# Kernel tuning notes

Hardware: AMD Instinct MI355X
Metric: run time of the kernel (lower is better)

Reference implementation:

```python
import jax, jax.numpy as jnp
import numpy as np

B, S, E, H = 2, 2048, 1024, 16
D = E // H  # head_dim
SCALE = 1.0 / np.sqrt(D)


def rope_tables(seq_len, dim, dtype=jnp.float32):
    # matches RotaryEmbedding: inv_freq over even indices, emb = cat([freqs, freqs])
    inv_freq = 1.0 / (10000.0 ** (jnp.arange(0, dim, 2, dtype=dtype) / dim))
    t = jnp.arange(seq_len, dtype=dtype)
    freqs = t[:, None] * inv_freq[None, :]          # [S, D/2]
    emb = jnp.concatenate([freqs, freqs], axis=-1)  # [S, D]
    return jnp.cos(emb)[None, None], jnp.sin(emb)[None, None]  # [1,1,S,D]


def apply_rope(x, cos, sin):
    # x: [B,H,S,D]; interleaved rotate exactly as the torch code:
    # x2 = stack([-x[...,1::2], x[...,0::2]], -1).reshape_as(x)
    x2 = jnp.stack([-x[..., 1::2], x[..., 0::2]], axis=-1).reshape(x.shape)
    return x * cos + x2 * sin


def setup_inputs() -> dict:
    key = jax.random.key(0)
    ks = jax.random.split(key, 12)
    std = 1.0 / np.sqrt(E)
    inp = {
        "query": jax.random.normal(ks[0], (B, S, E), jnp.float32),
        "key": jax.random.normal(ks[1], (B, S, E), jnp.float32),
        "value": jax.random.normal(ks[2], (B, S, E), jnp.float32),
        "mask": jnp.ones((B, S), jnp.int32),
        "Wq": jax.random.normal(ks[3], (E, E), jnp.float32) * std,
        "bq": jax.random.normal(ks[4], (E,), jnp.float32) * std,
        "Wk": jax.random.normal(ks[5], (E, E), jnp.float32) * std,
        "bk": jax.random.normal(ks[6], (E,), jnp.float32) * std,
        "Wv": jax.random.normal(ks[7], (E, E), jnp.float32) * std,
        "bv": jax.random.normal(ks[8], (E,), jnp.float32) * std,
        "Wo": jax.random.normal(ks[9], (E, E), jnp.float32) * std,
        "bo": jax.random.normal(ks[10], (E,), jnp.float32) * std,
    }
    return inp


def reference(query, key, value, mask, Wq, bq, Wk, bk, Wv, bv, Wo, bo):
    b, sq, _ = query.shape
    sk = key.shape[1]
    # linear projections (torch Linear: x @ W.T + b), split into heads [B,H,S,D]
    Q = (query @ Wq.T + bq).reshape(b, sq, H, D).transpose(0, 2, 1, 3)
    K = (key @ Wk.T + bk).reshape(b, sk, H, D).transpose(0, 2, 1, 3)
    V = (value @ Wv.T + bv).reshape(b, sk, H, D).transpose(0, 2, 1, 3)
    cos_q, sin_q = rope_tables(sq, D)
    cos_k, sin_k = rope_tables(sk, D)
    Q = apply_rope(Q, cos_q, sin_q)
    K = apply_rope(K, cos_k, sin_k)
    scores = jnp.einsum("bhqd,bhkd->bhqk", Q, K) * SCALE
    neg_inf = jnp.finfo(scores.dtype).min
    scores = jnp.where(mask[:, None, None, :] == 0, neg_inf, scores)
    attn = jax.nn.softmax(scores, axis=-1)
    # dropout omitted (deterministic reference / eval mode)
    out = jnp.einsum("bhqk,bhkd->bhqd", attn, V)
    out = out.transpose(0, 2, 1, 3).reshape(b, sq, E)
    return out @ Wo.T + bo
```

## Files before the change

### kernel.cpp

```cpp
#include <hip/hip_runtime.h>
#include <stdint.h>

typedef unsigned short u16;
typedef __bf16 bf16x8 __attribute__((ext_vector_type(8)));
typedef float f32x4 __attribute__((ext_vector_type(4)));
typedef float f32x2 __attribute__((ext_vector_type(2)));
typedef u16 u16x4v __attribute__((ext_vector_type(4)));

#define DI __device__ __forceinline__

constexpr int BB = 2, SS = 2048, EE = 1024, HH = 16, DD = 64;
constexpr int MROWS = BB * SS;
constexpr int KDIM = 1024, NDIM = 1024;

constexpr float FM = 12.0f;
constexpr float MNEG = -30000.f;

DI u16 f2bf(float f) {
  uint32_t u = __float_as_uint(f);
  return (u16)((u + 0x7FFFu + ((u >> 16) & 1u)) >> 16);
}
DI float bf2f(u16 h) { return __uint_as_float(((uint32_t)h) << 16); }

DI uint32_t cvtpk_bf16(float a, float b) {
  uint32_t r;
  asm("v_cvt_pk_bf16_f32 %0, %1, %2" : "=v"(r) : "v"(a), "v"(b));
  return r;
}

DI void cp16(const void* g, void* lds) {
  __builtin_amdgcn_global_load_lds((const __attribute__((address_space(1))) void*)g,
                                   (__attribute__((address_space(3))) void*)lds, 16, 0, 0);
}

DI f32x4 mfma16(bf16x8 a, bf16x8 b, f32x4 c) {
  return __builtin_amdgcn_mfma_f32_16x16x32_bf16(a, b, c, 0, 0, 0);
}

__global__ __launch_bounds__(256) void prep_cast(
    const float* __restrict__ q, const float* __restrict__ k, const float* __restrict__ v,
    const float* __restrict__ wq, const float* __restrict__ wk, const float* __restrict__ wv,
    const float* __restrict__ wo,
    u16* __restrict__ qb, u16* __restrict__ kb, u16* __restrict__ vb,
    u16* __restrict__ wqb, u16* __restrict__ wkb, u16* __restrict__ wvb,
    u16* __restrict__ wob) {
  constexpr size_t SZI = (size_t)MROWS * EE;
  constexpr size_t SZW = (size_t)EE * EE;
  const size_t g = ((size_t)blockIdx.x * 256 + threadIdx.x) * 4;
  const float* src; u16* dst; size_t o;
  if (g < SZI)          { src = q; dst = qb; o = g; }
  else if (g < 2 * SZI) { src = k; dst = kb; o = g - SZI; }
  else if (g < 3 * SZI) { src = v; dst = vb; o = g - 2 * SZI; }
  else {
    size_t t2 = g - 3 * SZI;
    int wi = (int)(t2 / SZW);
    o = t2 - (size_t)(wi < 4 ? wi : 3) * SZW;
    src = wi == 0 ? wq : wi == 1 ? wk : wi == 2 ? wv : wo;
    dst = wi == 0 ? wqb : wi == 1 ? wkb : wi == 2 ? wvb : wob;
  }
  const float4 f = *(const float4*)(src + o);
  u16x4v hv;
  hv[0] = f2bf(f.x); hv[1] = f2bf(f.y); hv[2] = f2bf(f.z); hv[3] = f2bf(f.w);
  *(u16x4v*)(dst + o) = hv;
}

__global__ __launch_bounds__(256) void rope_tables_k(float* __restrict__ csT,
                                                     const int* __restrict__ mask,
                                                     float* __restrict__ mfl) {
  const int t = blockIdx.x * 256 + threadIdx.x;
  const int s = t >> 6, d = t & 63, j = d & 31;
  const float ang = (float)s * exp2f(-(float)j * 0.4152410118f);
  float2 cs; cs.x = cosf(ang); cs.y = sinf(ang);
  ((float2*)csT)[t] = cs;
  if (t < BB * SS) mfl[t] = mask[t] ? -FM : MNEG;
}

__global__ __launch_bounds__(256) void gemm_qkv(
    const u16* __restrict__ qb, const u16* __restrict__ kb, const u16* __restrict__ vb,
    const u16* __restrict__ wqb, const u16* __restrict__ wkb, const u16* __restrict__ wvb,
    const float* __restrict__ bq, const float* __restrict__ bk, const float* __restrict__ bv,
    u16* __restrict__ Qp, u16* __restrict__ Kp, u16* __restrict__ Vtg,
    const float* __restrict__ csT) {
  __shared__ alignas(16) u16 sA[2][128 * 64];
  __shared__ alignas(16) u16 sB[2][128 * 64];
  const int tsel = blockIdx.y >> 5;
  const bool vtr = (tsel == 2);
  const u16* A    = tsel == 0 ? wqb : tsel == 1 ? wkb : vb;
  const u16* Bm   = tsel == 0 ? qb  : tsel == 1 ? kb  : wvb;
  const float* bias = tsel == 0 ? bq : tsel == 1 ? bk : bv;

  const int fBase = blockIdx.x * 128;
  const int tBase = (blockIdx.y & 31) * 128;
  const int aBase = vtr ? tBase : fBase;
  const int bBase = vtr ? fBase : tBase;
  const int tid = threadIdx.x;
  const int lane = tid & 63, w = tid >> 6;
  const int quad = lane >> 4, l16 = lane & 15;
  const int wr = w >> 1, wc = w & 1;

  size_t aSrc[4], bSrc[4];
  int dOff[4];
#pragma unroll
  for (int j = 0; j < 4; ++j) {
    const int c = tid + j * 256;
    const int row = c >> 3, sl = c & 7;
    const size_t off = (size_t)row * KDIM + ((sl ^ (row & 7)) * 8);
    aSrc[j] = (size_t)aBase * KDIM + off;
    bSrc[j] = (size_t)bBase * KDIM + off;
    dOff[j] = c * 8;
  }

  f32x4 acc[4][4];
#pragma unroll
  for (int mi = 0; mi < 4; ++mi)
#pragma unroll
    for (int ni = 0; ni < 4; ++ni)
#pragma unroll
      for (int e = 0; e < 4; ++e) acc[mi][ni][e] = 0.f;

  const int arow = wr * 64 + l16, brow = wc * 64 + l16;

  auto stage = [&](int k0, int bi) {
#pragma unroll
    for (int j = 0; j < 4; ++j) {
      cp16(A + aSrc[j] + k0, &sA[bi][dOff[j]]);
      cp16(Bm + bSrc[j] + k0, &sB[bi][dOff[j]]);
    }
  };

  stage(0, 0);
  __syncthreads();
  int buf = 0;
  for (int k0 = 0; k0 < KDIM; k0 += 64) {
    if (k0 + 64 < KDIM) stage(k0 + 64, buf ^ 1);
    __builtin_amdgcn_s_setprio(1);
#pragma unroll
    for (int h = 0; h < 2; ++h) {
      bf16x8 af[4], bf[4];
#pragma unroll
      for (int i = 0; i < 4; ++i) {
        const int ar = arow + i * 16, br = brow + i * 16;
        af[i] = *(const bf16x8*)&sA[buf][ar * 64 + (((h * 4 + quad) ^ (ar & 7)) << 3)];
        bf[i] = *(const bf16x8*)&sB[buf][br * 64 + (((h * 4 + quad) ^ (br & 7)) << 3)];
      }
#pragma unroll
      for (int mi = 0; mi < 4; ++mi)
#pragma unroll
        for (int ni = 0; ni < 4; ++ni)
          acc[mi][ni] = mfma16(af[mi], bf[ni], acc[mi][ni]);
    }
    __builtin_amdgcn_s_setprio(0);
    __syncthreads();
    buf ^= 1;
  }

  if (!vtr) {
    u16* C = tsel == 0 ? Qp : Kp;
#pragma unroll
    for (int mi = 0; mi < 4; ++mi) {
      const int fm = fBase + wr * 64 + mi * 16 + quad * 4;
      const float4 b4 = *(const float4*)&bias[fm];
      const int d0 = fm & 63;
#pragma unroll
      for (int ni = 0; ni < 4; ++ni) {
        const int t = tBase + wc * 64 + ni * 16 + l16;
        const int srow = t & (SS - 1);
        const float* cs = &csT[(size_t)((srow << 6) + d0) * 2];
        const float4 cs01 = *(const float4*)cs;
        const float4 cs23 = *(const float4*)(cs + 4);
        const float v0 = acc[mi][ni][0] + b4.x;
        const float v1 = acc[mi][ni][1] + b4.y;
        const float v2 = acc[mi][ni][2] + b4.z;
        const float v3 = acc[mi][ni][3] + b4.w;
        const float o0 = v0 * cs01.x - v1 * cs01.y;
        const float o1 = v1 * cs01.z + v0 * cs01.w;
        const float o2 = v2 * cs23.x - v3 * cs23.y;
        const float o3 = v3 * cs23.z + v2 * cs23.w;
        uint2 pk;
        pk.x = cvtpk_bf16(o0, o1);
        pk.y = cvtpk_bf16(o2, o3);
        *(uint2*)&C[(size_t)t * NDIM + fm] = pk;
      }
    }
  } else {
#pragma unroll
    for (int ni = 0; ni < 4; ++ni) {
      const int f = fBase + wc * 64 + ni * 16 + l16;
      const int h = f >> 6, d = f & 63;
      const float bb = bias[f];
#pragma unroll
      for (int mi = 0; mi < 4; ++mi) {
        const int t0 = tBase + wr * 64 + mi * 16 + quad * 4;
        const int b = t0 >> 11, s0 = t0 & (SS - 1);
        const int sp0 = (s0 & ~31) | (((s0 >> 2) & 3) << 3) | (((s0 >> 4) & 1) << 2);
        uint2 pk;
        pk.x = cvtpk_bf16(acc[mi][ni][0] + bb, acc[mi][ni][1] + bb);
        pk.y = cvtpk_bf16(acc[mi][ni][2] + bb, acc[mi][ni][3] + bb);
        *(uint2*)&Vtg[((size_t)((b * 16 + h) * 64 + d)) * SS + sp0] = pk;
      }
    }
  }
}

__global__ __launch_bounds__(512, 4) void attn_kernel(
    const u16* __restrict__ Qp, const u16* __restrict__ Kp, const u16* __restrict__ Vtg,
    const float* __restrict__ mfl, u16* __restrict__ Oh) {
  __shared__ alignas(16) u16 sK[2][128 * 64];
  __shared__ alignas(16) u16 sVt[2][64 * 128];
  __shared__ alignas(16) float sMaskAll[SS];
  const int tid = threadIdx.x, lane = tid & 63, w = tid >> 6;
  const int quad = lane >> 4, l16 = lane & 15;
  const int bh = blockIdx.y, b = bh >> 4, h = bh & 15;
  const int q0 = blockIdx.x * 128 + w * 16;
  const u16* Qb = Qp + (size_t)b * SS * EE + h * DD;
  const u16* Kb = Kp + (size_t)b * SS * EE + h * DD;
  const u16* Vb = Vtg + (size_t)bh * DD * SS;
  constexpr float C1 = 0.18033688011112042f;

  bf16x8 qf[2];
#pragma unroll
  for (int ks = 0; ks < 2; ++ks)
    qf[ks] = *(const bf16x8*)(Qb + (size_t)(q0 + l16) * EE + ks * 32 + quad * 8);

  f32x4 oacc[4];
#pragma unroll
  for (int nd = 0; nd < 4; ++nd)
#pragma unroll
    for (int e = 0; e < 4; ++e) oacc[nd][e] = 0.f;
  f32x2 sum2 = {0.f, 0.f};

  auto stage = [&](int kt, int bi) {
    const int key0 = kt * 128;
#pragma unroll
    for (int i = 0; i < 2; ++i) {
      const int c = i * 512 + tid;
      const int key = c >> 3;
      const int g8 = ((c & 7) ^ (key & 7)) * 8;
      cp16(Kb + (size_t)(key0 + key) * EE + g8, &sK[bi][c * 8]);
    }
#pragma unroll
    for (int i = 0; i < 2; ++i) {
      const int L = i * 512 + tid;
      const int d = L >> 4;
      const int g8 = ((L & 15) ^ (d & 15)) * 8;
      cp16(Vb + (size_t)d * SS + key0 + g8, &sVt[bi][L * 8]);
    }
  };

  auto compute = [&](int kt, int bi) {
    const int key0 = kt * 128;
    f32x4 sacc[8];
#pragma unroll
    for (int ni = 0; ni < 8; ++ni)
#pragma unroll
      for (int e = 0; e < 4; ++e) sacc[ni][e] = 0.f;
    __builtin_amdgcn_s_setprio(1);
#pragma unroll
    for (int ks = 0; ks < 2; ++ks)
#pragma unroll
      for (int ni = 0; ni < 8; ++ni) {
        const int row = ni * 16 + l16;
        const bf16x8 kf = *(const bf16x8*)&sK[bi][row * 64 + (((ks * 4 + quad) ^ (l16 & 7)) << 3)];
        sacc[ni] = mfma16(kf, qf[ks], sacc[ni]);
      }
    __builtin_amdgcn_s_setprio(0);

    uint32_t pw32[4][4];
#pragma unroll
    for (int ni = 0; ni < 8; ++ni) {
      const int kb4 = key0 + ni * 16 + quad * 4;
      const f32x2 m01 = *(const f32x2*)&sMaskAll[kb4];
      const f32x2 m23 = *(const f32x2*)&sMaskAll[kb4 + 2];
      f32x2 t01, t23;
      t01.x = sacc[ni][0]; t01.y = sacc[ni][1];
      t23.x = sacc[ni][2]; t23.y = sacc[ni][3];
      t01 = t01 * C1 + m01;
      t23 = t23 * C1 + m23;
      f32x2 p01, p23;
      p01.x = __builtin_amdgcn_exp2f(t01.x); p01.y = __builtin_amdgcn_exp2f(t01.y);
      p23.x = __builtin_amdgcn_exp2f(t23.x); p23.y = __builtin_amdgcn_exp2f(t23.y);
      sum2 += p01;
      sum2 += p23;
      const int k2 = ni >> 1, j2 = (ni & 1) * 2;
      pw32[k2][j2]     = cvtpk_bf16(p01.x, p01.y);
      pw32[k2][j2 + 1] = cvtpk_bf16(p23.x, p23.y);
    }

    __builtin_amdgcn_s_setprio(1);
#pragma unroll
    for (int k2 = 0; k2 < 4; ++k2) {
      union { uint32_t u[4]; bf16x8 v; } pf;
#pragma unroll
      for (int j = 0; j < 4; ++j) pf.u[j] = pw32[k2][j];
#pragma unroll
      for (int nd = 0; nd < 4; ++nd) {
        const int row = nd * 16 + l16;
        const bf16x8 vf = *(const bf16x8*)&sVt[bi][row * 128 + (((k2 * 4 + quad) ^ l16) << 3)];
        oacc[nd] = mfma16(pf.v, vf, oacc[nd]);
      }
    }
    __builtin_amdgcn_s_setprio(0);
  };

  stage(0, 0);
  cp16(mfl + (size_t)b * SS + tid * 4, &sMaskAll[tid * 4]);
  __syncthreads();

  for (int kt = 0; kt < SS / 128; kt += 2) {
    if (kt + 1 < SS / 128) stage(kt + 1, 1);
    compute(kt, 0);
    __syncthreads();
    if (kt + 2 < SS / 128) stage(kt + 2, 0);
    compute(kt + 1, 1);
    __syncthreads();
  }

  float lrow = sum2.x + sum2.y;
  lrow += __shfl_xor(lrow, 16, 64);
  lrow += __shfl_xor(lrow, 32, 64);
  const float linv = lrow > 0.f ? 1.0f / lrow : 0.f;

#pragma unroll
  for (int r = 0; r < 4; ++r) {
    const float li = __shfl(linv, quad * 4 + r, 16);
    const size_t row = (size_t)(b * SS + q0 + quad * 4 + r) * EE + h * DD;
#pragma unroll
    for (int nd = 0; nd < 4; ++nd) {
      const int d = nd * 16 + l16;
      Oh[row + d] = f2bf(oacc[nd][r] * li);
    }
  }
}

__global__ __launch_bounds__(256) void gemm_out(
    const u16* __restrict__ Ab, const u16* __restrict__ Bb,
    const float* __restrict__ bias, float* __restrict__ Cout) {
  __shared__ alignas(16) u16 sA[2][128 * 64];
  __shared__ alignas(16) u16 sB[2][64 * 64];
  const int rowBase = blockIdx.y * 128;
  const int colBase = blockIdx.x * 64;
  const int tid = threadIdx.x;
  const int lane = tid & 63, w = tid >> 6;
  const int quad = lane >> 4, l16 = lane & 15;
  const int wr = w >> 1, wc = w & 1;

  size_t aSrc[4]; int aOff[4];
  size_t bSrc[2]; int bOff[2];
#pragma unroll
  for (int j = 0; j < 4; ++j) {
    const int c = tid + j * 256;
    const int row = c >> 3, sl = c & 7;
    aSrc[j] = (size_t)(rowBase + row) * KDIM + ((sl ^ (row & 7)) * 8);
    aOff[j] = c * 8;
  }
#pragma unroll
  for (int j = 0; j < 2; ++j) {
    const int c = tid + j * 256;
    const int row = c >> 3, sl = c & 7;
    bSrc[j] = (size_t)(colBase + row) * KDIM + ((sl ^ (row & 7)) * 8);
    bOff[j] = c * 8;
  }

  f32x4 acc[4][2];
#pragma unroll
  for (int mi = 0; mi < 4; ++mi)
#pragma unroll
    for (int ni = 0; ni < 2; ++ni)
#pragma unroll
      for (int e = 0; e < 4; ++e) acc[mi][ni][e] = 0.f;

  const int arow = wr * 64 + l16, brow = wc * 32 + l16;

  auto stage = [&](int k0, int bi) {
#pragma unroll
    for (int j = 0; j < 4; ++j) cp16(Ab + aSrc[j] + k0, &sA[bi][aOff[j]]);
#pragma unroll
    for (int j = 0; j < 2; ++j) cp16(Bb + bSrc[j] + k0, &sB[bi][bOff[j]]);
  };

  stage(0, 0);
  __syncthreads();
  int buf = 0;
  for (int k0 = 0; k0 < KDIM; k0 += 64) {
    if (k0 + 64 < KDIM) stage(k0 + 64, buf ^ 1);
    __builtin_amdgcn_s_setprio(1);
#pragma unroll
    for (int h = 0; h < 2; ++h) {
      bf16x8 af[4], bf[2];
#pragma unroll
      for (int i = 0; i < 4; ++i) {
        const int ar = arow + i * 16;
        af[i] = *(const bf16x8*)&sA[buf][ar * 64 + (((h * 4 + quad) ^ (ar & 7)) << 3)];
      }
#pragma unroll
      for (int i = 0; i < 2; ++i) {
        const int br = brow + i * 16;
        bf[i] = *(const bf16x8*)&sB[buf][br * 64 + (((h * 4 + quad) ^ (br & 7)) << 3)];
      }
#pragma unroll
      for (int mi = 0; mi < 4; ++mi)
#pragma unroll
        for (int ni = 0; ni < 2; ++ni)
          acc[mi][ni] = mfma16(af[mi], bf[ni], acc[mi][ni]);
    }
    __builtin_amdgcn_s_setprio(0);
    __syncthreads();
    buf ^= 1;
  }

#pragma unroll
  for (int mi = 0; mi < 4; ++mi) {
    const int rb = rowBase + wr * 64 + mi * 16 + quad * 4;
#pragma unroll
    for (int ni = 0; ni < 2; ++ni) {
      const int col = colBase + wc * 32 + ni * 16 + l16;
      const float bb = bias[col];
#pragma unroll
      for (int r = 0; r < 4; ++r)
        Cout[(size_t)(rb + r) * NDIM + col] = acc[mi][ni][r] + bb;
    }
  }
}

extern "C" void kernel_launch(void* const* d_in, const int* in_sizes, int n_in,
                              void* d_out, int out_size, void* d_ws, size_t ws_size,
                              hipStream_t stream) {
  const float* q    = (const float*)d_in[0];
  const float* k    = (const float*)d_in[1];
  const float* v    = (const float*)d_in[2];
  const int*   mask = (const int*)d_in[3];
  const float* Wq = (const float*)d_in[4];
  const float* bq = (const float*)d_in[5];
  const float* Wk = (const float*)d_in[6];
  const float* bk = (const float*)d_in[7];
  const float* Wv = (const float*)d_in[8];
  const float* bv = (const float*)d_in[9];
  const float* Wo = (const float*)d_in[10];
  const float* bo = (const float*)d_in[11];
  float* out = (float*)d_out;
  char* ws = (char*)d_ws;
  constexpr size_t MB = 1024 * 1024;
  u16* qb  = (u16*)(ws + 0 * MB);
  u16* kb  = (u16*)(ws + 8 * MB);
  u16* vb  = (u16*)(ws + 16 * MB);
  u16* wqb = (u16*)(ws + 24 * MB);
  u16* wkb = (u16*)(ws + 26 * MB);
  u16* wvb = (u16*)(ws + 28 * MB);
  u16* wob = (u16*)(ws + 30 * MB);
  u16* Qp  = (u16*)(ws + 32 * MB);
  u16* Kp  = (u16*)(ws + 40 * MB);
  u16* Vtg = (u16*)(ws + 48 * MB);
  u16* oh  = (u16*)(ws + 56 * MB);
  float* csT = (float*)(ws + 64 * MB);
  float* mfl = out;

  prep_cast<<<16384, 256, 0, stream>>>(q, k, v, Wq, Wk, Wv, Wo,
                                       qb, kb, vb, wqb, wkb, wvb, wob);
  rope_tables_k<<<512, 256, 0, stream>>>(csT, mask, mfl);
  gemm_qkv<<<dim3(8, 96), 256, 0, stream>>>(qb, kb, vb, wqb, wkb, wvb,
                                            bq, bk, bv, Qp, Kp, Vtg, csT);
  attn_kernel<<<dim3(16, 32), 512, 0, stream>>>(Qp, Kp, Vtg, mfl, oh);
  gemm_out<<<dim3(16, 32), 256, 0, stream>>>(oh, wob, bo, out);
}
```

Measured before the change: 229.5 us.

## Give each attention wave two query tiles to reuse K/V shared-memory fragments

The attention kernel now runs 4 waves of 256 threads per block instead of 8, and each wave handles 32 query rows (two 16-row MFMA tiles) instead of 16. Every K and V fragment read from shared memory feeds two MFMAs, which halves LDS read traffic per unit of math and raises MFMA density per wave. In exchange each thread holds more registers (two sets of score and output accumulators), the launch bound drops to 2 blocks, and fewer waves per block are available to hide memory latency.

```diff
diff --git a/kernel.cpp b/kernel.cpp
--- a/kernel.cpp
+++ b/kernel.cpp
@@ -202,7 +202,7 @@
   }
 }
 
-__global__ __launch_bounds__(512, 4) void attn_kernel(
+__global__ __launch_bounds__(256, 2) void attn_kernel(
     const u16* __restrict__ Qp, const u16* __restrict__ Kp, const u16* __restrict__ Vtg,
     const float* __restrict__ mfl, u16* __restrict__ Oh) {
   __shared__ alignas(16) u16 sK[2][128 * 64];
@@ -211,36 +211,41 @@
   const int tid = threadIdx.x, lane = tid & 63, w = tid >> 6;
   const int quad = lane >> 4, l16 = lane & 15;
   const int bh = blockIdx.y, b = bh >> 4, h = bh & 15;
-  const int q0 = blockIdx.x * 128 + w * 16;
+  const int q0 = blockIdx.x * 128 + w * 32;
   const u16* Qb = Qp + (size_t)b * SS * EE + h * DD;
   const u16* Kb = Kp + (size_t)b * SS * EE + h * DD;
   const u16* Vb = Vtg + (size_t)bh * DD * SS;
   constexpr float C1 = 0.18033688011112042f;
 
-  bf16x8 qf[2];
-#pragma unroll
-  for (int ks = 0; ks < 2; ++ks)
-    qf[ks] = *(const bf16x8*)(Qb + (size_t)(q0 + l16) * EE + ks * 32 + quad * 8);
-
-  f32x4 oacc[4];
-#pragma unroll
-  for (int nd = 0; nd < 4; ++nd)
-#pragma unroll
-    for (int e = 0; e < 4; ++e) oacc[nd][e] = 0.f;
-  f32x2 sum2 = {0.f, 0.f};
+  bf16x8 qf[2][2];
+#pragma unroll
+  for (int qi = 0; qi < 2; ++qi)
+#pragma unroll
+    for (int ks = 0; ks < 2; ++ks)
+      qf[qi][ks] = *(const bf16x8*)(Qb + (size_t)(q0 + qi * 16 + l16) * EE + ks * 32 + quad * 8);
+
+  f32x4 oacc[2][4];
+#pragma unroll
+  for (int qi = 0; qi < 2; ++qi)
+#pragma unroll
+    for (int nd = 0; nd < 4; ++nd)
+#pragma unroll
+      for (int e = 0; e < 4; ++e) oacc[qi][nd][e] = 0.f;
+  f32x2 sum2[2];
+  sum2[0] = {0.f, 0.f}; sum2[1] = {0.f, 0.f};
 
   auto stage = [&](int kt, int bi) {
     const int key0 = kt * 128;
 #pragma unroll
-    for (int i = 0; i < 2; ++i) {
-      const int c = i * 512 + tid;
+    for (int i = 0; i < 4; ++i) {
+      const int c = i * 256 + tid;
       const int key = c >> 3;
       const int g8 = ((c & 7) ^ (key & 7)) * 8;
       cp16(Kb + (size_t)(key0 + key) * EE + g8, &sK[bi][c * 8]);
     }
 #pragma unroll
-    for (int i = 0; i < 2; ++i) {
-      const int L = i * 512 + tid;
+    for (int i = 0; i < 4; ++i) {
+      const int L = i * 256 + tid;
       const int d = L >> 4;
       const int g8 = ((L & 15) ^ (d & 15)) * 8;
       cp16(Vb + (size_t)d * SS + key0 + g8, &sVt[bi][L * 8]);
@@ -249,11 +254,13 @@
 
   auto compute = [&](int kt, int bi) {
     const int key0 = kt * 128;
-    f32x4 sacc[8];
-#pragma unroll
-    for (int ni = 0; ni < 8; ++ni)
-#pragma unroll
-      for (int e = 0; e < 4; ++e) sacc[ni][e] = 0.f;
+    f32x4 sacc[2][8];
+#pragma unroll
+    for (int qi = 0; qi < 2; ++qi)
+#pragma unroll
+      for (int ni = 0; ni < 8; ++ni)
+#pragma unroll
+        for (int e = 0; e < 4; ++e) sacc[qi][ni][e] = 0.f;
     __builtin_amdgcn_s_setprio(1);
 #pragma unroll
     for (int ks = 0; ks < 2; ++ks)
@@ -261,49 +268,61 @@
       for (int ni = 0; ni < 8; ++ni) {
         const int row = ni * 16 + l16;
         const bf16x8 kf = *(const bf16x8*)&sK[bi][row * 64 + (((ks * 4 + quad) ^ (l16 & 7)) << 3)];
-        sacc[ni] = mfma16(kf, qf[ks], sacc[ni]);
+#pragma unroll
+        for (int qi = 0; qi < 2; ++qi)
+          sacc[qi][ni] = mfma16(kf, qf[qi][ks], sacc[qi][ni]);
       }
     __builtin_amdgcn_s_setprio(0);
 
-    uint32_t pw32[4][4];
-#pragma unroll
-    for (int ni = 0; ni < 8; ++ni) {
-      const int kb4 = key0 + ni * 16 + quad * 4;
-      const f32x2 m01 = *(const f32x2*)&sMaskAll[kb4];
-      const f32x2 m23 = *(const f32x2*)&sMaskAll[kb4 + 2];
-      f32x2 t01, t23;
-      t01.x = sacc[ni][0]; t01.y = sacc[ni][1];
-      t23.x = sacc[ni][2]; t23.y = sacc[ni][3];
-      t01 = t01 * C1 + m01;
-      t23 = t23 * C1 + m23;
-      f32x2 p01, p23;
-      p01.x = __builtin_amdgcn_exp2f(t01.x); p01.y = __builtin_amdgcn_exp2f(t01.y);
-      p23.x = __builtin_amdgcn_exp2f(t23.x); p23.y = __builtin_amdgcn_exp2f(t23.y);
-      sum2 += p01;
-      sum2 += p23;
-      const int k2 = ni >> 1, j2 = (ni & 1) * 2;
-      pw32[k2][j2]     = cvtpk_bf16(p01.x, p01.y);
-      pw32[k2][j2 + 1] = cvtpk_bf16(p23.x, p23.y);
-    }
+    uint32_t pw32[2][4][4];
+#pragma unroll
+    for (int qi = 0; qi < 2; ++qi)
+#pragma unroll
+      for (int ni = 0; ni < 8; ++ni) {
+        const int kb4 = key0 + ni * 16 + quad * 4;
+        const f32x2 m01 = *(const f32x2*)&sMaskAll[kb4];
+        const f32x2 m23 = *(const f32x2*)&sMaskAll[kb4 + 2];
+        f32x2 t01, t23;
+        t01.x = sacc[qi][ni][0]; t01.y = sacc[qi][ni][1];
+        t23.x = sacc[qi][ni][2]; t23.y = sacc[qi][ni][3];
+        t01 = t01 * C1 + m01;
+        t23 = t23 * C1 + m23;
+        f32x2 p01, p23;
+        p01.x = __builtin_amdgcn_exp2f(t01.x); p01.y = __builtin_amdgcn_exp2f(t01.y);
+        p23.x = __builtin_amdgcn_exp2f(t23.x); p23.y = __builtin_amdgcn_exp2f(t23.y);
+        sum2[qi] += p01;
+        sum2[qi] += p23;
+        const int k2 = ni >> 1, j2 = (ni & 1) * 2;
+        pw32[qi][k2][j2]     = cvtpk_bf16(p01.x, p01.y);
+        pw32[qi][k2][j2 + 1] = cvtpk_bf16(p23.x, p23.y);
+      }
 
     __builtin_amdgcn_s_setprio(1);
 #pragma unroll
     for (int k2 = 0; k2 < 4; ++k2) {
-      union { uint32_t u[4]; bf16x8 v; } pf;
-#pragma unroll
-      for (int j = 0; j < 4; ++j) pf.u[j] = pw32[k2][j];
+      union { uint32_t u[4]; bf16x8 v; } pf[2];
+#pragma unroll
+      for (int qi = 0; qi < 2; ++qi)
+#pragma unroll
+        for (int j = 0; j < 4; ++j) pf[qi].u[j] = pw32[qi][k2][j];
 #pragma unroll
       for (int nd = 0; nd < 4; ++nd) {
         const int row = nd * 16 + l16;
         const bf16x8 vf = *(const bf16x8*)&sVt[bi][row * 128 + (((k2 * 4 + quad) ^ l16) << 3)];
-        oacc[nd] = mfma16(pf.v, vf, oacc[nd]);
+#pragma unroll
+        for (int qi = 0; qi < 2; ++qi)
+          oacc[qi][nd] = mfma16(pf[qi].v, vf, oacc[qi][nd]);
       }
     }
     __builtin_amdgcn_s_setprio(0);
   };
 
   stage(0, 0);
-  cp16(mfl + (size_t)b * SS + tid * 4, &sMaskAll[tid * 4]);
+#pragma unroll
+  for (int i = 0; i < 2; ++i) {
+    const int t4 = (i * 256 + tid) * 4;
+    cp16(mfl + (size_t)b * SS + t4, &sMaskAll[t4]);
+  }
   __syncthreads();
 
   for (int kt = 0; kt < SS / 128; kt += 2) {
@@ -315,21 +334,27 @@
     __syncthreads();
   }
 
-  float lrow = sum2.x + sum2.y;
-  lrow += __shfl_xor(lrow, 16, 64);
-  lrow += __shfl_xor(lrow, 32, 64);
-  const float linv = lrow > 0.f ? 1.0f / lrow : 0.f;
-
-#pragma unroll
-  for (int r = 0; r < 4; ++r) {
-    const float li = __shfl(linv, quad * 4 + r, 16);
-    const size_t row = (size_t)(b * SS + q0 + quad * 4 + r) * EE + h * DD;
-#pragma unroll
-    for (int nd = 0; nd < 4; ++nd) {
-      const int d = nd * 16 + l16;
-      Oh[row + d] = f2bf(oacc[nd][r] * li);
-    }
-  }
+  float linv[2];
+#pragma unroll
+  for (int qi = 0; qi < 2; ++qi) {
+    float lrow = sum2[qi].x + sum2[qi].y;
+    lrow += __shfl_xor(lrow, 16, 64);
+    lrow += __shfl_xor(lrow, 32, 64);
+    linv[qi] = lrow > 0.f ? 1.0f / lrow : 0.f;
+  }
+
+#pragma unroll
+  for (int qi = 0; qi < 2; ++qi)
+#pragma unroll
+    for (int r = 0; r < 4; ++r) {
+      const float li = __shfl(linv[qi], quad * 4 + r, 16);
+      const size_t row = (size_t)(b * SS + q0 + qi * 16 + quad * 4 + r) * EE + h * DD;
+#pragma unroll
+      for (int nd = 0; nd < 4; ++nd) {
+        const int d = nd * 16 + l16;
+        Oh[row + d] = f2bf(oacc[qi][nd][r] * li);
+      }
+    }
 }
 
 __global__ __launch_bounds__(256) void gemm_out(
@@ -459,6 +484,6 @@
   rope_tables_k<<<512, 256, 0, stream>>>(csT, mask, mfl);
   gemm_qkv<<<dim3(8, 96), 256, 0, stream>>>(qb, kb, vb, wqb, wkb, wvb,
                                             bq, bk, bv, Qp, Kp, Vtg, csT);
-  attn_kernel<<<dim3(16, 32), 512, 0, stream>>>(Qp, Kp, Vtg, mfl, oh);
+  attn_kernel<<<dim3(16, 32), 256, 0, stream>>>(Qp, Kp, Vtg, mfl, oh);
   gemm_out<<<dim3(16, 32), 256, 0, stream>>>(oh, wob, bo, out);
 }
```

After: 231.1 us. Within noise of the previous version (+0.7%).
